# Kernel optimization log

Hardware: AMD Instinct MI355X
Metric: run time of the kernel (lower is better)

## Reference

```python
import jax, jax.numpy as jnp
import numpy as np

B, D, C = 512, 512, 100000
U_M, L_M, U_A, L_A = 0.8, 0.45, 110.0, 10.0
LAMBDA_G, SCALE = 35.0, 64.0


def setup_inputs() -> dict:
    key = jax.random.key(0)
    k1, k2, k3, k4 = jax.random.split(key, 4)
    x = jax.random.normal(k1, (B, D), dtype=jnp.float32)
    # magnitudes in [l_a, u_a] as in MagFace
    x_norm = L_A + (U_A - L_A) * jax.random.uniform(k2, (B,), dtype=jnp.float32)
    labels = jax.random.randint(k3, (B,), 0, C, dtype=jnp.int64)
    weight = jax.random.normal(k4, (C, D), dtype=jnp.float32)
    return {"x": x, "x_norm": x_norm, "labels": labels, "weight": weight}


def _l2norm(a, axis=-1, eps=1e-12):
    return a / jnp.maximum(jnp.linalg.norm(a, axis=axis, keepdims=True), eps)


def reference(x, x_norm, labels, weight):
    # adaptive margin per sample, shape [B]
    margin = (U_M - L_M) / (U_A - L_A) * (x_norm - L_A) + L_M

    # cos_theta = normalize(x) @ normalize(W).T  -> [B, C]
    cos_theta = jnp.clip(_l2norm(x) @ _l2norm(weight).T, -1.0, 1.0)

    theta = jnp.arccos(cos_theta)
    valid = labels != -1  # [B]
    safe_labels = jnp.where(valid, labels, 0)
    # add margin at the target class (only for valid labels)
    add = jnp.where(valid, margin, 0.0)  # [B]
    theta = theta.at[jnp.arange(theta.shape[0]), safe_labels].add(add)

    logits = jnp.cos(theta) * SCALE  # [B, C]

    # cross-entropy, ignoring labels == -1
    lse = jax.nn.logsumexp(logits, axis=-1)  # [B]
    tgt = jnp.take_along_axis(logits, safe_labels[:, None], axis=-1)[:, 0]
    nll = jnp.where(valid, lse - tgt, 0.0)
    n_valid = jnp.maximum(jnp.sum(valid.astype(jnp.float32)), 1.0)
    ce = jnp.sum(nll) / n_valid

    # MagFace G-loss
    g_loss = jnp.mean(x_norm / (U_A * U_A) + 1.0 / x_norm)

    return ce + LAMBDA_G * g_loss
```

## Files before the change

### kernel.cpp

```cpp
#include <hip/hip_runtime.h>

typedef unsigned short u16;
typedef unsigned int u32;
typedef float f32x4 __attribute__((ext_vector_type(4)));
typedef short bf16x8 __attribute__((ext_vector_type(8)));

#define U_M 0.8f
#define L_M 0.45f
#define U_A 110.0f
#define L_A 10.0f
#define LAMBDA_G 35.0f
#define SCALEF 64.0f

__device__ __forceinline__ u16 f2bf(float f) {
  u32 u = __builtin_bit_cast(u32, f);
  u32 r = (u + 0x7fffu + ((u >> 16) & 1u)) >> 16;
  return (u16)r;
}

__device__ __forceinline__ u32 cvtpk(float lo, float hi) {
  u32 r;
  asm("v_cvt_pk_bf16_f32 %0, %1, %2" : "=v"(r) : "v"(lo), "v"(hi));
  return r;
}

__global__ void xnorm_kernel(const float* __restrict__ x, u16* __restrict__ xn, int K) {
  int row = blockIdx.x * 4 + (threadIdx.x >> 6);
  int l = threadIdx.x & 63;
  const float4* p = reinterpret_cast<const float4*>(x + (size_t)row * K) + l * 2;
  float4 a = p[0], b = p[1];
  float s = a.x*a.x + a.y*a.y + a.z*a.z + a.w*a.w
          + b.x*b.x + b.y*b.y + b.z*b.z + b.w*b.w;
  #pragma unroll
  for (int m = 32; m >= 1; m >>= 1) s += __shfl_xor(s, m);
  float inv = rsqrtf(fmaxf(s, 1e-24f));
  u32 q0 = (u32)f2bf(a.x*inv) | ((u32)f2bf(a.y*inv) << 16);
  u32 q1 = (u32)f2bf(a.z*inv) | ((u32)f2bf(a.w*inv) << 16);
  u32 q2 = (u32)f2bf(b.x*inv) | ((u32)f2bf(b.y*inv) << 16);
  u32 q3 = (u32)f2bf(b.z*inv) | ((u32)f2bf(b.w*inv) << 16);
  *reinterpret_cast<uint4*>(xn + (size_t)row * K + l * 8) = make_uint4(q0, q1, q2, q3);
}

__global__ void tgt_kernel(const float* __restrict__ x, const float* __restrict__ W,
                           const int* __restrict__ labels, float* __restrict__ tgtcos, int K) {
  int b = blockIdx.x;
  int l = threadIdx.x;
  int lab = labels[b];
  int labc = lab < 0 ? 0 : lab;
  const float4* px = reinterpret_cast<const float4*>(x + (size_t)b * K) + l * 2;
  const float4* pw = reinterpret_cast<const float4*>(W + (size_t)labc * K) + l * 2;
  float4 a0 = px[0], a1 = px[1], w0 = pw[0], w1 = pw[1];
  float dot = a0.x*w0.x + a0.y*w0.y + a0.z*w0.z + a0.w*w0.w
            + a1.x*w1.x + a1.y*w1.y + a1.z*w1.z + a1.w*w1.w;
  float sx = a0.x*a0.x + a0.y*a0.y + a0.z*a0.z + a0.w*a0.w
           + a1.x*a1.x + a1.y*a1.y + a1.z*a1.z + a1.w*a1.w;
  float sw = w0.x*w0.x + w0.y*w0.y + w0.z*w0.z + w0.w*w0.w
           + w1.x*w1.x + w1.y*w1.y + w1.z*w1.z + w1.w*w1.w;
  #pragma unroll
  for (int m = 32; m >= 1; m >>= 1) {
    dot += __shfl_xor(dot, m);
    sx  += __shfl_xor(sx, m);
    sw  += __shfl_xor(sw, m);
  }
  if (l == 0) {
    float cv = dot * rsqrtf(fmaxf(sx, 1e-24f)) * rsqrtf(fmaxf(sw, 1e-24f));
    tgtcos[b] = fminf(fmaxf(cv, -1.f), 1.f);
  }
}

__global__ __launch_bounds__(512, 4) void gemm_wf32(
    const u16* __restrict__ xn, const float* __restrict__ W,
    const int* __restrict__ labels,
    float* __restrict__ partials, int C, int K, int M) {
  __shared__ u16 sA[128 * 64];
  __shared__ u16 sB[128 * 64];
  __shared__ float bsum[4][128];
  __shared__ float sIw[128];
  __shared__ int slab[128];

  int nwg = gridDim.x;
  int id = blockIdx.x;
  int q = nwg >> 3, r = nwg & 7;
  int xcd = id & 7, pos = id >> 3;
  int wg = (xcd < r ? xcd * (q + 1) : r * (q + 1) + (xcd - r) * q) + pos;
  const int bm = wg & 3, bn = wg >> 2;

  const int t = threadIdx.x;
  const int l = t & 63, wid = t >> 6;
  const int wm = wid >> 2, wn_ = wid & 3;
  const int n0 = bn * 128;
  if (t < 128) slab[t] = labels[bm * 128 + t];

  const int qq = t & 3;
  const int rbase = t >> 2;
  const int rc = (n0 + rbase) < C ? (n0 + rbase) : C - 1;
  const float* wp = W + (size_t)rc * K + qq * 16;
  float ssq = 0.f;

  f32x4 acc[4][2] = {};
  const int nkt = K >> 6;
  for (int kt = 0; kt < nkt; ++kt) {
    const int k0 = kt << 6;

    float4 v[4];
    {
      const float4* p = reinterpret_cast<const float4*>(wp + k0);
      #pragma unroll
      for (int j = 0; j < 4; ++j) v[j] = p[j];
    }

    #pragma unroll
    for (int i = 0; i < 2; ++i) {
      int L = i * 512 + t;
      int rr = L >> 3;
      int cs = (L & 7) ^ (rr & 7);
      const u16* src = xn + (size_t)(bm * 128 + rr) * K + k0 + cs * 8;
      __builtin_amdgcn_global_load_lds(
          (const __attribute__((address_space(1))) void*)src,
          (__attribute__((address_space(3))) void*)(sA + (size_t)(i * 512 + (t & 448)) * 8),
          16, 0, 0);
    }

    {
      float s = 0.f;
      u32 pk[8];
      #pragma unroll
      for (int j = 0; j < 4; ++j) {
        float4 f = v[j];
        s += f.x*f.x + f.y*f.y + f.z*f.z + f.w*f.w;
        pk[j*2]   = cvtpk(f.x, f.y);
        pk[j*2+1] = cvtpk(f.z, f.w);
      }
      ssq += s;
      int c0 = qq * 2;
      *reinterpret_cast<uint4*>(sB + rbase * 64 + (((c0    ) ^ (rbase & 7)) * 8)) = make_uint4(pk[0], pk[1], pk[2], pk[3]);
      *reinterpret_cast<uint4*>(sB + rbase * 64 + (((c0 + 1) ^ (rbase & 7)) * 8)) = make_uint4(pk[4], pk[5], pk[6], pk[7]);
    }

    __syncthreads();
    #pragma unroll
    for (int ks = 0; ks < 2; ++ks) {
      bf16x8 af[4], bfr[2];
      #pragma unroll
      for (int mi = 0; mi < 4; ++mi) {
        int row = wm * 64 + mi * 16 + (l & 15);
        int ch = ks * 4 + (l >> 4);
        af[mi] = *reinterpret_cast<const bf16x8*>(sA + row * 64 + ((ch ^ (row & 7)) * 8));
      }
      #pragma unroll
      for (int ni = 0; ni < 2; ++ni) {
        int row = wn_ * 32 + ni * 16 + (l & 15);
        int ch = ks * 4 + (l >> 4);
        bfr[ni] = *reinterpret_cast<const bf16x8*>(sB + row * 64 + ((ch ^ (row & 7)) * 8));
      }
      #pragma unroll
      for (int mi = 0; mi < 4; ++mi)
        #pragma unroll
        for (int ni = 0; ni < 2; ++ni)
          acc[mi][ni] = __builtin_amdgcn_mfma_f32_16x16x32_bf16(af[mi], bfr[ni], acc[mi][ni], 0, 0, 0);
    }
    __syncthreads();
  }

  {
    float s0 = ssq + __shfl_xor(ssq, 1);
    s0 += __shfl_xor(s0, 2);
    if (qq == 0) sIw[rbase] = rsqrtf(fmaxf(s0, 1e-24f));
  }
  __syncthreads();

  float iw[2]; int colv[2];
  #pragma unroll
  for (int ni = 0; ni < 2; ++ni) {
    int cl = wn_ * 32 + ni * 16 + (l & 15);
    colv[ni] = n0 + cl;
    iw[ni] = sIw[cl];
  }
  #pragma unroll
  for (int mi = 0; mi < 4; ++mi) {
    #pragma unroll
    for (int rg = 0; rg < 4; ++rg) {
      int row_l = wm * 64 + mi * 16 + ((l >> 4) << 2) + rg;
      int labr = slab[row_l];
      float rs = 0.f;
      #pragma unroll
      for (int ni = 0; ni < 2; ++ni) {
        float cv = acc[mi][ni][rg] * iw[ni];
        cv = fminf(fmaxf(cv, -1.f), 1.f);
        float e = __expf(SCALEF * cv - SCALEF);
        bool keep = (colv[ni] < C) && (colv[ni] != labr);
        rs += keep ? e : 0.f;
      }
      rs += __shfl_xor(rs, 1);
      rs += __shfl_xor(rs, 2);
      rs += __shfl_xor(rs, 4);
      rs += __shfl_xor(rs, 8);
      if ((l & 15) == 0) bsum[wn_][row_l] = rs;
    }
  }
  __syncthreads();
  if (t < 128) {
    partials[(size_t)bn * M + bm * 128 + t] =
        (bsum[0][t] + bsum[1][t]) + (bsum[2][t] + bsum[3][t]);
  }
}

__global__ void rowreduce_kernel(const float* __restrict__ partials, float* __restrict__ rowsum,
                                 int NBN, int M) {
  int b = blockIdx.x, t = threadIdx.x;
  float s = 0.f;
  for (int i = t; i < NBN; i += 256) s += partials[(size_t)i * M + b];
  __shared__ float sh[256];
  sh[t] = s; __syncthreads();
  for (int off = 128; off >= 1; off >>= 1) {
    if (t < off) sh[t] += sh[t + off];
    __syncthreads();
  }
  if (t == 0) rowsum[b] = sh[0];
}

__global__ void final_kernel(const float* __restrict__ rowsum, const float* __restrict__ tgtcos,
                             const float* __restrict__ x_norm, const int* __restrict__ labels,
                             float* __restrict__ out, int Bn) {
  int t = threadIdx.x;
  float nll = 0.f, g = 0.f, vld = 0.f;
  if (t < Bn) {
    float a = x_norm[t];
    g = a * (1.0f / (U_A * U_A)) + 1.0f / a;
    int lab = labels[t];
    bool valid = (lab != -1);
    if (valid) {
      float ct = tgtcos[t];
      float margin = ((U_M - L_M) / (U_A - L_A)) * (a - L_A) + L_M;
      float theta = acosf(ct) + margin;
      float tl = SCALEF * cosf(theta);
      float se = rowsum[t] + __expf(tl - SCALEF);
      float lse = SCALEF + logf(se);
      nll = lse - tl;
      vld = 1.f;
    }
  }
  __shared__ float s1[512], s2[512], s3[512];
  s1[t] = nll; s2[t] = g; s3[t] = vld;
  __syncthreads();
  for (int off = 256; off >= 1; off >>= 1) {
    if (t < off) { s1[t] += s1[t + off]; s2[t] += s2[t + off]; s3[t] += s3[t + off]; }
    __syncthreads();
  }
  if (t == 0) {
    float ce = s1[0] / fmaxf(s3[0], 1.f);
    out[0] = ce + LAMBDA_G * (s2[0] / (float)Bn);
  }
}

extern "C" void kernel_launch(void* const* d_in, const int* in_sizes, int n_in,
                              void* d_out, int out_size, void* d_ws, size_t ws_size,
                              hipStream_t stream) {
  const float* x      = (const float*)d_in[0];
  const float* x_norm = (const float*)d_in[1];
  const int*   labels = (const int*)d_in[2];
  const float* W      = (const float*)d_in[3];
  float* out = (float*)d_out;

  const int B = in_sizes[1];
  const int D = in_sizes[0] / B;
  const int C = in_sizes[3] / D;
  const int NBN = (C + 127) / 128;

  char* ws = (char*)d_ws;
  size_t o_xn   = 0;
  size_t o_tgt  = o_xn + (size_t)B * D * 2;
  size_t o_rows = o_tgt + (size_t)B * 4;
  size_t o_part = o_rows + (size_t)B * 4;

  u16*   xn       = (u16*)(ws + o_xn);
  float* tgtcos   = (float*)(ws + o_tgt);
  float* rowsum   = (float*)(ws + o_rows);
  float* partials = (float*)(ws + o_part);

  hipLaunchKernelGGL(xnorm_kernel, dim3(B / 4), dim3(256), 0, stream, x, xn, D);
  hipLaunchKernelGGL(tgt_kernel, dim3(B), dim3(64), 0, stream, x, W, labels, tgtcos, D);
  hipLaunchKernelGGL(gemm_wf32, dim3(NBN * (B / 128)), dim3(512), 0, stream,
                     xn, W, labels, partials, C, D, B);
  hipLaunchKernelGGL(rowreduce_kernel, dim3(B), dim3(256), 0, stream, partials, rowsum, NBN, B);
  hipLaunchKernelGGL(final_kernel, dim3(1), dim3(B), 0, stream, rowsum, tgtcos, x_norm, labels, out, B);
}
```

Before: 129.9 us.

## Software-pipeline GEMM K-loop with double-buffered A tile and coalesced W loads

Restructures the K loop so the next tile's fp32 W rows are loaded into registers and the next bf16 xn tile is fetched into a second LDS buffer while MFMAs run on the current tile. The W load mapping changes from 4 threads per row with 64-byte strides to 16 threads per row across 4 row groups, giving contiguous per-row float4 accesses, and the per-row sum-of-squares reduction widens accordingly. This aims to hide global load latency of the memory-bound fp32 weight stream. It costs extra LDS for the second A buffer, more registers, and an extra barrier per iteration, which could lower occupancy.

```diff
diff --git a/kernel.cpp b/kernel.cpp
--- a/kernel.cpp
+++ b/kernel.cpp
@@ -72,7 +72,7 @@
     const u16* __restrict__ xn, const float* __restrict__ W,
     const int* __restrict__ labels,
     float* __restrict__ partials, int C, int K, int M) {
-  __shared__ u16 sA[128 * 64];
+  __shared__ u16 sA[2][128 * 64];
   __shared__ u16 sB[128 * 64];
   __shared__ float bsum[4][128];
   __shared__ float sIw[128];
@@ -91,53 +91,66 @@
   const int n0 = bn * 128;
   if (t < 128) slab[t] = labels[bm * 128 + t];
 
-  const int qq = t & 3;
-  const int rbase = t >> 2;
-  const int rc = (n0 + rbase) < C ? (n0 + rbase) : C - 1;
-  const float* wp = W + (size_t)rc * K + qq * 16;
-  float ssq = 0.f;
+  const int c4 = t & 15;
+  const int rowL = t >> 4;
+  const float* wp[4];
+  #pragma unroll
+  for (int p = 0; p < 4; ++p) {
+    int rr = n0 + p * 32 + rowL;
+    rr = rr < C ? rr : C - 1;
+    wp[p] = W + (size_t)rr * K + c4 * 4;
+  }
+  float ssq[4] = {0.f, 0.f, 0.f, 0.f};
+
+  const int nkt = K >> 6;
+  float4 v[4];
+
+  #pragma unroll
+  for (int p = 0; p < 4; ++p) v[p] = *reinterpret_cast<const float4*>(wp[p]);
+  #pragma unroll
+  for (int i = 0; i < 2; ++i) {
+    int L = i * 512 + t;
+    int rr = L >> 3;
+    int cs = (L & 7) ^ (rr & 7);
+    const u16* src = xn + (size_t)(bm * 128 + rr) * K + cs * 8;
+    __builtin_amdgcn_global_load_lds(
+        (const __attribute__((address_space(1))) void*)src,
+        (__attribute__((address_space(3))) void*)(sA[0] + (size_t)(i * 512 + (t & 448)) * 8),
+        16, 0, 0);
+  }
+  #pragma unroll
+  for (int p = 0; p < 4; ++p) {
+    float4 f = v[p];
+    ssq[p] += f.x*f.x + f.y*f.y + f.z*f.z + f.w*f.w;
+    int rr = p * 32 + rowL;
+    uint2 pk = make_uint2(cvtpk(f.x, f.y), cvtpk(f.z, f.w));
+    *reinterpret_cast<uint2*>(sB + rr * 64 + (((c4 >> 1) ^ (rr & 7)) * 8) + (c4 & 1) * 4) = pk;
+  }
+  __syncthreads();
 
   f32x4 acc[4][2] = {};
-  const int nkt = K >> 6;
   for (int kt = 0; kt < nkt; ++kt) {
-    const int k0 = kt << 6;
-
-    float4 v[4];
-    {
-      const float4* p = reinterpret_cast<const float4*>(wp + k0);
-      #pragma unroll
-      for (int j = 0; j < 4; ++j) v[j] = p[j];
-    }
-
-    #pragma unroll
-    for (int i = 0; i < 2; ++i) {
-      int L = i * 512 + t;
-      int rr = L >> 3;
-      int cs = (L & 7) ^ (rr & 7);
-      const u16* src = xn + (size_t)(bm * 128 + rr) * K + k0 + cs * 8;
-      __builtin_amdgcn_global_load_lds(
-          (const __attribute__((address_space(1))) void*)src,
-          (__attribute__((address_space(3))) void*)(sA + (size_t)(i * 512 + (t & 448)) * 8),
-          16, 0, 0);
-    }
-
-    {
-      float s = 0.f;
-      u32 pk[8];
-      #pragma unroll
-      for (int j = 0; j < 4; ++j) {
-        float4 f = v[j];
-        s += f.x*f.x + f.y*f.y + f.z*f.z + f.w*f.w;
-        pk[j*2]   = cvtpk(f.x, f.y);
-        pk[j*2+1] = cvtpk(f.z, f.w);
-      }
-      ssq += s;
-      int c0 = qq * 2;
-      *reinterpret_cast<uint4*>(sB + rbase * 64 + (((c0    ) ^ (rbase & 7)) * 8)) = make_uint4(pk[0], pk[1], pk[2], pk[3]);
-      *reinterpret_cast<uint4*>(sB + rbase * 64 + (((c0 + 1) ^ (rbase & 7)) * 8)) = make_uint4(pk[4], pk[5], pk[6], pk[7]);
-    }
-
-    __syncthreads();
+    const bool pf = (kt + 1) < nkt;
+    const u16* aCur = sA[kt & 1];
+
+    if (pf) {
+      const int k1 = (kt + 1) << 6;
+      #pragma unroll
+      for (int p = 0; p < 4; ++p) v[p] = *reinterpret_cast<const float4*>(wp[p] + k1);
+      u16* aNxt = sA[(kt + 1) & 1];
+      #pragma unroll
+      for (int i = 0; i < 2; ++i) {
+        int L = i * 512 + t;
+        int rr = L >> 3;
+        int cs = (L & 7) ^ (rr & 7);
+        const u16* src = xn + (size_t)(bm * 128 + rr) * K + k1 + cs * 8;
+        __builtin_amdgcn_global_load_lds(
+            (const __attribute__((address_space(1))) void*)src,
+            (__attribute__((address_space(3))) void*)(aNxt + (size_t)(i * 512 + (t & 448)) * 8),
+            16, 0, 0);
+      }
+    }
+
     #pragma unroll
     for (int ks = 0; ks < 2; ++ks) {
       bf16x8 af[4], bfr[2];
@@ -145,7 +158,7 @@
       for (int mi = 0; mi < 4; ++mi) {
         int row = wm * 64 + mi * 16 + (l & 15);
         int ch = ks * 4 + (l >> 4);
-        af[mi] = *reinterpret_cast<const bf16x8*>(sA + row * 64 + ((ch ^ (row & 7)) * 8));
+        af[mi] = *reinterpret_cast<const bf16x8*>(aCur + row * 64 + ((ch ^ (row & 7)) * 8));
       }
       #pragma unroll
       for (int ni = 0; ni < 2; ++ni) {
@@ -159,13 +172,30 @@
         for (int ni = 0; ni < 2; ++ni)
           acc[mi][ni] = __builtin_amdgcn_mfma_f32_16x16x32_bf16(af[mi], bfr[ni], acc[mi][ni], 0, 0, 0);
     }
+
     __syncthreads();
-  }
-
-  {
-    float s0 = ssq + __shfl_xor(ssq, 1);
-    s0 += __shfl_xor(s0, 2);
-    if (qq == 0) sIw[rbase] = rsqrtf(fmaxf(s0, 1e-24f));
+
+    if (pf) {
+      #pragma unroll
+      for (int p = 0; p < 4; ++p) {
+        float4 f = v[p];
+        ssq[p] += f.x*f.x + f.y*f.y + f.z*f.z + f.w*f.w;
+        int rr = p * 32 + rowL;
+        uint2 pk = make_uint2(cvtpk(f.x, f.y), cvtpk(f.z, f.w));
+        *reinterpret_cast<uint2*>(sB + rr * 64 + (((c4 >> 1) ^ (rr & 7)) * 8) + (c4 & 1) * 4) = pk;
+      }
+    }
+    __syncthreads();
+  }
+
+  #pragma unroll
+  for (int p = 0; p < 4; ++p) {
+    float s = ssq[p];
+    s += __shfl_xor(s, 1);
+    s += __shfl_xor(s, 2);
+    s += __shfl_xor(s, 4);
+    s += __shfl_xor(s, 8);
+    if (c4 == 0) sIw[p * 32 + rowL] = rsqrtf(fmaxf(s, 1e-24f));
   }
   __syncthreads();
 
```

New measurement: 124.4 us. 4.2% less time.
